# Optimization experiments

Hardware: AMD Instinct MI355X
Metric: run time of the kernel (lower is better)

Reference implementation:

```python
import jax, jax.numpy as jnp
import numpy as np

N, M, B = 2048, 2048, 1
D, H, DQK, DV = 1024, 16, 64, 64
OFFSET = 0
PARAM_SCALE = 0.02  # keeps logits in a sane range (original uses plain randn)


def setup_inputs() -> dict:
    key = jax.random.key(0)
    ks = jax.random.split(key, 7)
    return {
        "x_q": jax.random.normal(ks[0], (N, B, D), jnp.float32),
        "x_kv": jax.random.normal(ks[1], (M, B, D), jnp.float32),
        "to_q": jax.random.normal(ks[2], (DQK, H, D), jnp.float32) * PARAM_SCALE,
        "to_k": jax.random.normal(ks[3], (DQK, H, D), jnp.float32) * PARAM_SCALE,
        "to_v": jax.random.normal(ks[4], (DV, H, D), jnp.float32) * PARAM_SCALE,
        "to_out": jax.random.normal(ks[5], (D, DV, H), jnp.float32) * PARAM_SCALE,
        "for_pos_enc": jax.random.normal(ks[6], (DQK, H, D), jnp.float32) * PARAM_SCALE,
    }


def _sincos(n, m, offset, d_x_kv, dtype):
    # relative distances i - j + offset range over [offset-(m-1), offset+(n-1)]
    r = jnp.arange(offset - (m - 1), offset + (n - 1) + 1, dtype=dtype)  # [R], R=n+m-1
    inv_freq = 1.0 / (10000.0 ** (jnp.arange(0.0, d_x_kv, 2.0, dtype=dtype) / d_x_kv))
    phases = r[:, None] * inv_freq[None, :]  # [R, d/2]
    return jnp.concatenate([jnp.sin(phases), jnp.cos(phases)], axis=-1)  # [R, d]


def reference(x_q, x_kv, to_q, to_k, to_v, to_out, for_pos_enc):
    n, b, _ = x_q.shape
    m = x_kv.shape[0]
    # q: [n, d_qk, b, h]
    q = jnp.einsum('dhb,nab->ndah', to_q, x_q)
    # content logits: [n, m, b, h]
    k = jnp.einsum('dhc,mac->mdah', to_k, x_kv)
    content = jnp.einsum('ndah,mdah->nmah', q, k)
    # relative positional encoding (same math as pos_enc[dists - min] then einsum,
    # but logits computed per relative position then gathered -> no [n,m,d,h] blowup)
    sincos = _sincos(n, m, OFFSET, x_kv.shape[-1], x_q.dtype)  # [R, d_x_kv]
    pe_rel = jnp.einsum('dhb,rb->rdh', for_pos_enc, sincos)    # [R, d_qk, h]
    pl_rel = jnp.einsum('ndah,rdh->nrah', q, pe_rel)            # [n, R, b, h]
    idx = jnp.arange(n)[:, None] - jnp.arange(m)[None, :] + (m - 1)  # dists - dists.min()
    position = pl_rel[jnp.arange(n)[:, None], idx]               # [n, m, b, h]
    logits = content + position
    # causal mask: True above diagonal shifted by 1+offset
    mask = jnp.triu(jnp.ones((n, m), bool), 1 + OFFSET)
    logits = jnp.where(mask[:, :, None, None], -jnp.inf, logits)
    weights = jax.nn.softmax(logits, axis=1)                     # softmax over m
    v = jnp.einsum('chb,mab->mach', to_v, x_kv)                  # [m, b, dv, h]
    ctx = jnp.einsum('nmah,mach->nach', weights, v)              # [n, b, dv, h]
    out = jnp.einsum('dch,nach->nad', to_out, ctx)               # [n, b, d]
    return out
```

## Files before the change

kernel.cpp:

```cpp
#include <hip/hip_runtime.h>
#include <hip/hip_bf16.h>

#define N_Q   2048
#define M_KV  2048
#define DIM   1024
#define NH    16
#define DHEAD 64
#define KDIM  1024
#define PEROWS 2112
#define PEBUF  2176

typedef __attribute__((ext_vector_type(8))) __bf16 bf16x8;
typedef __attribute__((ext_vector_type(4))) float  f32x4;

typedef __attribute__((address_space(1))) const unsigned char gbyte_t;
typedef __attribute__((address_space(3))) unsigned char lbyte_t;

__device__ __forceinline__ unsigned short f2bf(float f) {
  union { float f; unsigned u; } v; v.f = f;
  unsigned u = v.u;
  u = u + 0x7fffu + ((u >> 16) & 1u);
  return (unsigned short)(u >> 16);
}

#define PREP_A 524288
#define PREP_B 1048576
#define PREP_C 2097152
#define PREP_D 2359296
#define PREP_E 2916352
__global__ __launch_bounds__(256) void prep_kernel(
    const float* __restrict__ x_q, const float* __restrict__ x_kv,
    const float* __restrict__ to_q, const float* __restrict__ to_k,
    const float* __restrict__ to_v, const float* __restrict__ to_pe,
    const float* __restrict__ to_out,
    unsigned short* __restrict__ xq_bf, unsigned short* __restrict__ xkv_bf,
    unsigned short* __restrict__ wq_bf, unsigned short* __restrict__ wkv_bf,
    unsigned short* __restrict__ wp_bf, unsigned short* __restrict__ wo_bf,
    unsigned short* __restrict__ sc_bf) {
  int gid = blockIdx.x * 256 + threadIdx.x;
  if (gid < PREP_B) {
    const float* src = (gid < PREP_A) ? x_q : x_kv;
    unsigned short* dst = (gid < PREP_A) ? xq_bf : xkv_bf;
    int e4 = (gid < PREP_A ? gid : gid - PREP_A) * 4;
    float4 v = *(const float4*)(src + e4);
    ushort4 o = { f2bf(v.x), f2bf(v.y), f2bf(v.z), f2bf(v.w) };
    *(ushort4*)(dst + e4) = o;
  } else if (gid < PREP_C) {
    int e = gid - PREP_B;
    int which = e >> 18, inner = e & 262143;
    int e4 = inner * 4;
    int j = e4 >> 10, b = e4 & 1023;
    int d = j & 63, h = j >> 6;
    const float* w = (which == 0) ? to_q : (which == 1) ? to_k : (which == 2) ? to_v : to_pe;
    unsigned short* o = (which == 0) ? wq_bf : (which == 1) ? wkv_bf
                       : (which == 2) ? (wkv_bf + (size_t)DIM * DIM) : wp_bf;
    float4 v = *(const float4*)(w + (size_t)(d * NH + h) * DIM + b);
    ushort4 u = { f2bf(v.x), f2bf(v.y), f2bf(v.z), f2bf(v.w) };
    *(ushort4*)(o + e4) = u;
  } else if (gid < PREP_D) {
    int e4 = (gid - PREP_C) * 4;
    int dd = e4 >> 10, jc = e4 & 1023;
    int c = jc & 63, h = jc >> 6;
    const float* base = to_out + (size_t)(dd * DHEAD + c) * NH + h;
    ushort4 u = { f2bf(base[0]), f2bf(base[16]), f2bf(base[32]), f2bf(base[48]) };
    *(ushort4*)(wo_bf + e4) = u;
  } else if (gid < PREP_E) {
    int e = gid - PREP_D;
    int r = e >> 8, t8 = e & 255;
    float ph0base = (float)(r - 63);
    unsigned short ss[2], cc[2];
    #pragma unroll
    for (int i = 0; i < 2; ++i) {
      int k2 = t8 * 2 + i;
      float invf = __expf((float)k2 * (-9.210340371976184f / 512.0f));
      float s, c;
      __sincosf(ph0base * invf, &s, &c);
      ss[i] = f2bf(s); cc[i] = f2bf(c);
    }
    unsigned short* row = sc_bf + (size_t)r * DIM;
    *(unsigned int*)(row + t8 * 2)       = (unsigned)ss[0] | ((unsigned)ss[1] << 16);
    *(unsigned int*)(row + t8 * 2 + 512) = (unsigned)cc[0] | ((unsigned)cc[1] << 16);
  }
}

__global__ __launch_bounds__(256) void gemm_in_kernel(
    const unsigned short* __restrict__ xq, const unsigned short* __restrict__ xkv,
    const unsigned short* __restrict__ sc,
    const unsigned short* __restrict__ wq, const unsigned short* __restrict__ wkv,
    const unsigned short* __restrict__ wp,
    unsigned short* __restrict__ qout, unsigned short* __restrict__ kout,
    unsigned short* __restrict__ vtout, unsigned short* __restrict__ peout) {
  int bid0 = (int)blockIdx.x;
  int bid  = (bid0 & 7) * 130 + (bid0 >> 3);
  const unsigned short *A, *B; unsigned short *C1, *C2;
  int Mr, maxBrow, mode, ax, by;
  if (bid < 256)      { int t = bid;       ax = t & 15; by = t >> 4; A = xq;  B = wq;  C1 = qout;  C2 = nullptr; Mr = N_Q;    maxBrow = DIM - 1;     mode = 1; }
  else if (bid < 768) { int t = bid - 256; ax = t & 15; by = t >> 4; A = xkv; B = wkv; C1 = kout;  C2 = vtout;   Mr = M_KV;   maxBrow = 2 * DIM - 1; mode = 3; }
  else                { int t = bid - 768; ax = t % 17; by = t / 17; A = sc;  B = wp;  C1 = peout; C2 = nullptr; Mr = PEROWS; maxBrow = DIM - 1;     mode = 1; }

  __shared__ unsigned short As[2][128][64];
  __shared__ unsigned short Bs[2][64][64];
  int tid  = threadIdx.x;
  int wave = tid >> 6, lane = tid & 63;
  int g = lane >> 4, r16 = lane & 15;
  int arow0 = ax * 128;
  int brow0 = by * 64;
  int amax  = Mr - 1;

  auto stage = [&](int buf, int kt) {
    #pragma unroll
    for (int n = 0; n < 4; ++n) {
      int seg  = wave * 4 + n;
      int rloc = seg * 8 + (lane >> 3);
      int cbyte = ((lane & 7) << 4) ^ ((rloc & 7) << 4);
      int grow = min(arow0 + rloc, amax);
      const unsigned short* gp = A + (size_t)grow * KDIM + kt + (cbyte >> 1);
      __builtin_amdgcn_global_load_lds((gbyte_t*)(const void*)gp,
                                       (lbyte_t*)(void*)&As[buf][seg * 8][0], 16, 0, 0);
    }
    #pragma unroll
    for (int n = 0; n < 2; ++n) {
      int seg  = wave * 2 + n;
      int rloc = seg * 8 + (lane >> 3);
      int cbyte = ((lane & 7) << 4) ^ ((rloc & 7) << 4);
      int grow = min(brow0 + rloc, maxBrow);
      const unsigned short* gp = B + (size_t)grow * KDIM + kt + (cbyte >> 1);
      __builtin_amdgcn_global_load_lds((gbyte_t*)(const void*)gp,
                                       (lbyte_t*)(void*)&Bs[buf][seg * 8][0], 16, 0, 0);
    }
  };

  f32x4 acc[2][4];
  #pragma unroll
  for (int i = 0; i < 2; ++i)
    #pragma unroll
    for (int j = 0; j < 4; ++j) acc[i][j] = (f32x4){0,0,0,0};

  stage(0, 0);
  asm volatile("s_waitcnt vmcnt(0)" ::: "memory");
  __syncthreads();

  int buf = 0;
  for (int t = 0; t < 16; ++t) {
    if (t < 15) stage(buf ^ 1, (t + 1) * 64);

    bf16x8 af[2][2], bfr[4][2];
    #pragma unroll
    for (int i = 0; i < 2; ++i)
      #pragma unroll
      for (int kk = 0; kk < 2; ++kk) {
        int r = wave * 32 + i * 16 + r16;
        int cb = ((kk << 6) | (g << 4)) ^ ((r & 7) << 4);
        af[i][kk] = *(const bf16x8*)((const char*)&As[buf][r][0] + cb);
      }
    #pragma unroll
    for (int j = 0; j < 4; ++j)
      #pragma unroll
      for (int kk = 0; kk < 2; ++kk) {
        int r = j * 16 + r16;
        int cb = ((kk << 6) | (g << 4)) ^ ((r & 7) << 4);
        bfr[j][kk] = *(const bf16x8*)((const char*)&Bs[buf][r][0] + cb);
      }
    __builtin_amdgcn_s_setprio(1);
    #pragma unroll
    for (int kk = 0; kk < 2; ++kk)
      #pragma unroll
      for (int i = 0; i < 2; ++i)
        #pragma unroll
        for (int j = 0; j < 4; ++j)
          acc[i][j] = __builtin_amdgcn_mfma_f32_16x16x32_bf16(af[i][kk], bfr[j][kk], acc[i][j], 0, 0, 0);
    __builtin_amdgcn_s_setprio(0);

    if (t < 15) {
      asm volatile("s_waitcnt vmcnt(0)" ::: "memory");
      __syncthreads();
      buf ^= 1;
    }
  }

  #pragma unroll
  for (int i = 0; i < 2; ++i)
    #pragma unroll
    for (int j = 0; j < 4; ++j)
      #pragma unroll
      for (int rr = 0; rr < 4; ++rr) {
        int row = arow0 + wave * 32 + i * 16 + g * 4 + rr;
        int col = brow0 + j * 16 + r16;
        float v = acc[i][j][rr];
        if (mode == 1) {
          if (row < Mr) C1[(size_t)row * 1024 + col] = f2bf(v);
        } else {
          if (col < 1024) C1[(size_t)row * 1024 + col] = f2bf(v);
          else            C2[(size_t)(col - 1024) * M_KV + row] = f2bf(v);
        }
      }
}

__global__ __launch_bounds__(256) void gemm_out_kernel(
    const unsigned short* __restrict__ A, const unsigned short* __restrict__ B,
    float* __restrict__ C1) {
  __shared__ unsigned short As[2][64][64];
  __shared__ unsigned short Bs[2][64][64];
  int tid  = threadIdx.x;
  int wave = tid >> 6, lane = tid & 63;
  int wr = wave >> 1, wc = wave & 1;
  int g = lane >> 4, r16 = lane & 15;
  int arow0 = blockIdx.x * 64;
  int brow0 = blockIdx.y * 64;

  auto stage = [&](int buf, int kt) {
    #pragma unroll
    for (int n = 0; n < 2; ++n) {
      int seg  = wave * 2 + n;
      int rloc = seg * 8 + (lane >> 3);
      int cbyte = ((lane & 7) << 4) ^ ((rloc & 7) << 4);
      const unsigned short* gpA = A + (size_t)(arow0 + rloc) * KDIM + kt + (cbyte >> 1);
      __builtin_amdgcn_global_load_lds((gbyte_t*)(const void*)gpA,
                                       (lbyte_t*)(void*)&As[buf][seg * 8][0], 16, 0, 0);
      const unsigned short* gpB = B + (size_t)(brow0 + rloc) * KDIM + kt + (cbyte >> 1);
      __builtin_amdgcn_global_load_lds((gbyte_t*)(const void*)gpB,
                                       (lbyte_t*)(void*)&Bs[buf][seg * 8][0], 16, 0, 0);
    }
  };

  f32x4 acc[2][2] = {{{0,0,0,0},{0,0,0,0}},{{0,0,0,0},{0,0,0,0}}};

  stage(0, 0);
  asm volatile("s_waitcnt vmcnt(0)" ::: "memory");
  __syncthreads();

  int buf = 0;
  for (int t = 0; t < 16; ++t) {
    if (t < 15) stage(buf ^ 1, (t + 1) * 64);
    bf16x8 af[2][2], bfr[2][2];
    #pragma unroll
    for (int i = 0; i < 2; ++i)
      #pragma unroll
      for (int kk = 0; kk < 2; ++kk) {
        int r = wr * 32 + i * 16 + r16;
        int cb = ((kk << 6) | (g << 4)) ^ ((r & 7) << 4);
        af[i][kk] = *(const bf16x8*)((const char*)&As[buf][r][0] + cb);
      }
    #pragma unroll
    for (int j = 0; j < 2; ++j)
      #pragma unroll
      for (int kk = 0; kk < 2; ++kk) {
        int r = wc * 32 + j * 16 + r16;
        int cb = ((kk << 6) | (g << 4)) ^ ((r & 7) << 4);
        bfr[j][kk] = *(const bf16x8*)((const char*)&Bs[buf][r][0] + cb);
      }
    __builtin_amdgcn_s_setprio(1);
    #pragma unroll
    for (int kk = 0; kk < 2; ++kk)
      #pragma unroll
      for (int i = 0; i < 2; ++i)
        #pragma unroll
        for (int j = 0; j < 2; ++j)
          acc[i][j] = __builtin_amdgcn_mfma_f32_16x16x32_bf16(af[i][kk], bfr[j][kk], acc[i][j], 0, 0, 0);
    __builtin_amdgcn_s_setprio(0);
    if (t < 15) {
      asm volatile("s_waitcnt vmcnt(0)" ::: "memory");
      __syncthreads();
      buf ^= 1;
    }
  }

  #pragma unroll
  for (int i = 0; i < 2; ++i)
    #pragma unroll
    for (int j = 0; j < 2; ++j)
      #pragma unroll
      for (int rr = 0; rr < 4; ++rr) {
        int row = arow0 + wr * 32 + i * 16 + g * 4 + rr;
        int col = brow0 + wc * 32 + j * 16 + r16;
        C1[(size_t)row * 1024 + col] = acc[i][j][rr];
      }
}

__global__ __launch_bounds__(256, 2) void attn_mfma_kernel(
    const unsigned short* __restrict__ qb, const unsigned short* __restrict__ kb,
    const unsigned short* __restrict__ vt, const unsigned short* __restrict__ pe,
    unsigned short* __restrict__ ctx, float* __restrict__ part) {
  int ord  = (int)blockIdx.x;
  int h    = ord & 15;
  int widx = 79 - (ord >> 4);
  int b, c;
  if (widx < 8)       { b = widx;                                  c = 0; }
  else if (widx < 24) { int t2 = widx - 8;  b = 8  + (t2 >> 1);    c = t2 & 1; }
  else if (widx < 48) { int t2 = widx - 24; int q3 = t2 / 3; b = 16 + q3; c = t2 - 3 * q3; }
  else                { int t2 = widx - 48; b = 24 + (t2 >> 2);    c = t2 & 3; }
  int n0   = b * 64;
  int nc   = (b < 8) ? 1 : (b >> 3) + 1;
  int t0   = c * 8;
  int tend = min(t0 + 8, b + 1);

  int wave = threadIdx.x >> 6;
  int lane = threadIdx.x & 63;
  int g    = lane >> 4;
  int r16  = lane & 15;

  __shared__ unsigned short Ks[2][64][64];
  __shared__ unsigned short Vs[2][64][64];
  __shared__ unsigned short PEs[2][128][64];
  __shared__ unsigned short W_lds[4][16][72];

  const unsigned short* qrow = qb + (size_t)(n0 + wave * 16 + r16) * DIM + h * 64 + g * 8;
  bf16x8 aq0 = *(const bf16x8*)(qrow);
  bf16x8 aq1 = *(const bf16x8*)(qrow + 32);

  union { unsigned short u[8]; bf16x8 v; } one_u;
  #pragma unroll
  for (int i = 0; i < 8; ++i) one_u.u[i] = 0x3F80;
  bf16x8 ones = one_u.v;

  f32x4 acc[4] = {{0,0,0,0},{0,0,0,0},{0,0,0,0},{0,0,0,0}};
  f32x4 lacc = {0,0,0,0};

  auto stage = [&](int bufn, int tilen) {
    int m0n = tilen * 64;
    int prb = n0 - m0n;
    #pragma unroll
    for (int n = 0; n < 2; ++n) {
      int seg  = wave * 2 + n;
      int rloc = seg * 8 + (lane >> 3);
      int cbyte = ((lane & 7) << 4) ^ ((rloc & 7) << 4);
      const unsigned short* gpk = kb + (size_t)(m0n + rloc) * KDIM + h * 64 + (cbyte >> 1);
      __builtin_amdgcn_global_load_lds((gbyte_t*)(const void*)gpk,
                                       (lbyte_t*)(void*)&Ks[bufn][seg * 8][0], 16, 0, 0);
      const unsigned short* gpv = vt + (size_t)(h * 64 + rloc) * M_KV + m0n + (cbyte >> 1);
      __builtin_amdgcn_global_load_lds((gbyte_t*)(const void*)gpv,
                                       (lbyte_t*)(void*)&Vs[bufn][seg * 8][0], 16, 0, 0);
    }
    #pragma unroll
    for (int n = 0; n < 4; ++n) {
      int seg  = wave * 4 + n;
      int rloc = seg * 8 + (lane >> 3);
      int cbyte = ((lane & 7) << 4) ^ ((rloc & 7) << 4);
      const unsigned short* gpp = pe + (size_t)(prb + rloc) * KDIM + h * 64 + (cbyte >> 1);
      __builtin_amdgcn_global_load_lds((gbyte_t*)(const void*)gpp,
                                       (lbyte_t*)(void*)&PEs[bufn][seg * 8][0], 16, 0, 0);
    }
  };

  int srcl[4]; bool hi_sel[4];
  #pragma unroll
  for (int rr = 0; rr < 4; ++rr) {
    srcl[rr]   = (g << 4) | ((g * 4 + rr + 63 - r16) & 15);
    hi_sel[rr] = (g * 4 + rr) > r16;
  }
  int sw = (r16 & 7) << 4;

  stage(0, t0);
  asm volatile("s_waitcnt vmcnt(0)" ::: "memory");
  __syncthreads();

  int buf = 0;
  for (int tile = t0; tile < tend; ++tile) {
    int m0 = tile * 64;
    if (tile + 1 < tend) stage(buf ^ 1, tile + 1);

    f32x4 s[4];
    __builtin_amdgcn_s_setprio(1);
    #pragma unroll
    for (int ct = 0; ct < 4; ++ct) {
      const char* kbase = (const char*)&Ks[buf][ct * 16 + r16][0];
      bf16x8 k0 = *(const bf16x8*)(kbase + (((g << 4)) ^ sw));
      bf16x8 k1 = *(const bf16x8*)(kbase + ((64 | (g << 4)) ^ sw));
      f32x4 z = {0,0,0,0};
      z = __builtin_amdgcn_mfma_f32_16x16x32_bf16(aq0, k0, z, 0, 0, 0);
      z = __builtin_amdgcn_mfma_f32_16x16x32_bf16(aq1, k1, z, 0, 0, 0);
      s[ct] = z;
    }

    f32x4 z2[5];
    #pragma unroll
    for (int cp = 0; cp < 5; ++cp) {
      const char* pbase = (const char*)&PEs[buf][wave * 16 + cp * 16 + r16][0];
      bf16x8 p0 = *(const bf16x8*)(pbase + (((g << 4)) ^ sw));
      bf16x8 p1 = *(const bf16x8*)(pbase + ((64 | (g << 4)) ^ sw));
      f32x4 z = {0,0,0,0};
      z = __builtin_amdgcn_mfma_f32_16x16x32_bf16(aq0, p0, z, 0, 0, 0);
      z = __builtin_amdgcn_mfma_f32_16x16x32_bf16(aq1, p1, z, 0, 0, 0);
      z2[cp] = z;
    }
    __builtin_amdgcn_s_setprio(0);

    bool diag = (m0 == n0);
    #pragma unroll
    for (int ct = 0; ct < 4; ++ct) {
      #pragma unroll
      for (int rr = 0; rr < 4; ++rr) {
        float vhi = __shfl(z2[4 - ct][rr], srcl[rr], 64);
        float vlo = __shfl(z2[3 - ct][rr], srcl[rr], 64);
        float p   = hi_sel[rr] ? vhi : vlo;
        int il = g * 4 + rr;
        int it = wave * 16 + il;
        int jt = ct * 16 + r16;
        float val = s[ct][rr] + p;
        if (diag && jt > it) val = -1e30f;
        s[ct][rr] = __expf(val);
      }
    }

    #pragma unroll
    for (int ct = 0; ct < 4; ++ct)
      #pragma unroll
      for (int rr = 0; rr < 4; ++rr)
        W_lds[wave][g * 4 + rr][ct * 16 + r16] = f2bf(s[ct][rr]);
    bf16x8 aw0 = *(const bf16x8*)(&W_lds[wave][r16][g * 8]);
    bf16x8 aw1 = *(const bf16x8*)(&W_lds[wave][r16][g * 8 + 32]);

    __builtin_amdgcn_s_setprio(1);
    #pragma unroll
    for (int ct = 0; ct < 4; ++ct) {
      const char* vbase = (const char*)&Vs[buf][ct * 16 + r16][0];
      bf16x8 v0 = *(const bf16x8*)(vbase + (((g << 4)) ^ sw));
      bf16x8 v1 = *(const bf16x8*)(vbase + ((64 | (g << 4)) ^ sw));
      f32x4 a = acc[ct];
      a = __builtin_amdgcn_mfma_f32_16x16x32_bf16(aw0, v0, a, 0, 0, 0);
      a = __builtin_amdgcn_mfma_f32_16x16x32_bf16(aw1, v1, a, 0, 0, 0);
      acc[ct] = a;
    }
    lacc = __builtin_amdgcn_mfma_f32_16x16x32_bf16(aw0, ones, lacc, 0, 0, 0);
    lacc = __builtin_amdgcn_mfma_f32_16x16x32_bf16(aw1, ones, lacc, 0, 0, 0);
    __builtin_amdgcn_s_setprio(0);

    asm volatile("s_waitcnt vmcnt(0)" ::: "memory");
    __syncthreads();
    buf ^= 1;
  }

  if (nc == 1) {
    #pragma unroll
    for (int rr = 0; rr < 4; ++rr) {
      float inv = 1.0f / lacc[rr];
      #pragma unroll
      for (int ct = 0; ct < 4; ++ct) {
        int row = n0 + wave * 16 + g * 4 + rr;
        ctx[(size_t)row * DIM + h * 64 + ct * 16 + r16] = f2bf(acc[ct][rr] * inv);
      }
    }
  } else {
    float* slot = part + ((size_t)((b - 8) * 16 + h) * 4 + c) * (64 * 68);
    #pragma unroll
    for (int ct = 0; ct < 4; ++ct)
      #pragma unroll
      for (int rr = 0; rr < 4; ++rr) {
        int row = wave * 16 + g * 4 + rr;
        slot[row * 68 + ct * 16 + r16] = acc[ct][rr];
      }
    if (r16 == 0) {
      #pragma unroll
      for (int rr = 0; rr < 4; ++rr) {
        int row = wave * 16 + g * 4 + rr;
        slot[row * 68 + 64] = lacc[rr];
      }
    }
  }
}

__global__ __launch_bounds__(256) void combine_kernel(const float* __restrict__ part,
                                                      unsigned short* __restrict__ ctx) {
  int bb = blockIdx.x;
  int h  = blockIdx.y;
  int b  = bb + 8;
  int nc = (b >> 3) + 1;
  int t  = threadIdx.x;
  int row = t >> 2, q = t & 3;
  const float* base = part + ((size_t)(bb * 16 + h) * 4) * (64 * 68) + row * 68;
  float lstar = 0.0f;
  for (int c2 = 0; c2 < nc; ++c2) lstar += base[c2 * 4352 + 64];
  float inv = 1.0f / lstar;
  for (int cc = 0; cc < 16; ++cc) {
    int col = q * 16 + cc;
    float o = 0.0f;
    for (int c2 = 0; c2 < nc; ++c2) o += base[c2 * 4352 + col];
    ctx[(size_t)(b * 64 + row) * DIM + h * 64 + col] = f2bf(o * inv);
  }
}

extern "C" void kernel_launch(void* const* d_in, const int* in_sizes, int n_in,
                              void* d_out, int out_size, void* d_ws, size_t ws_size,
                              hipStream_t stream) {
  const float* x_q    = (const float*)d_in[0];
  const float* x_kv   = (const float*)d_in[1];
  const float* to_q   = (const float*)d_in[2];
  const float* to_k   = (const float*)d_in[3];
  const float* to_v   = (const float*)d_in[4];
  const float* to_out = (const float*)d_in[5];
  const float* to_pe  = (const float*)d_in[6];

  char* ws = (char*)d_ws;
  size_t off = 0;
  auto alloc = [&](size_t bytes) -> char* {
    char* p = ws + off;
    off += (bytes + 255) & ~(size_t)255;
    return p;
  };

  unsigned short* xq_bf  = (unsigned short*)alloc((size_t)N_Q  * DIM * 2);
  unsigned short* xkv_bf = (unsigned short*)alloc((size_t)M_KV * DIM * 2);
  unsigned short* wq_bf  = (unsigned short*)alloc((size_t)DIM * DIM * 2);
  unsigned short* wkv_bf = (unsigned short*)alloc((size_t)2 * DIM * DIM * 2);
  unsigned short* wp_bf  = (unsigned short*)alloc((size_t)DIM * DIM * 2);
  unsigned short* wo_bf  = (unsigned short*)alloc((size_t)DIM * DIM * 2);
  unsigned short* sc_bf  = (unsigned short*)alloc((size_t)PEBUF * DIM * 2);
  unsigned short* q_bf   = (unsigned short*)alloc((size_t)N_Q  * DIM * 2);
  unsigned short* k_bf   = (unsigned short*)alloc((size_t)M_KV * DIM * 2);
  unsigned short* vt_bf  = (unsigned short*)alloc((size_t)DIM * M_KV * 2);
  unsigned short* pe_bf  = (unsigned short*)alloc((size_t)PEBUF * DIM * 2);
  unsigned short* ctx_bf = (unsigned short*)alloc((size_t)N_Q * DIM * 2);
  float*          part   = (float*)alloc((size_t)24 * 16 * 4 * 64 * 68 * 4);

  prep_kernel<<<11392, 256, 0, stream>>>(x_q, x_kv, to_q, to_k, to_v, to_pe, to_out,
                                         xq_bf, xkv_bf, wq_bf, wkv_bf, wp_bf, wo_bf, sc_bf);

  gemm_in_kernel<<<1040, 256, 0, stream>>>(xq_bf, xkv_bf, sc_bf, wq_bf, wkv_bf, wp_bf,
                                           q_bf, k_bf, vt_bf, pe_bf);

  attn_mfma_kernel<<<1280, 256, 0, stream>>>(q_bf, k_bf, vt_bf, pe_bf, ctx_bf, part);
  combine_kernel<<<dim3(24, NH), 256, 0, stream>>>(part, ctx_bf);

  gemm_out_kernel<<<dim3(32, 16), 256, 0, stream>>>(ctx_bf, wo_bf, (float*)d_out);
}
```

Measured before the change: 135.4 us.

## Triple-buffer LDS staging in input/output projection GEMMs with partial vmcnt waits

Both projection GEMM kernels move from double to triple buffered LDS staging, prefetching two K-tiles ahead. Waits become partial (vmcnt of one stage's loads still in flight) instead of draining all loads each iteration, and __syncthreads is replaced with a raw s_barrier plus a sched_barrier. The goal is to hide global-load latency behind MFMA work. In exchange LDS use per block grows by half, which may lower occupancy. Correctness depends on the vmcnt counts matching the number of loads issued per stage.

```diff
diff --git a/kernel.cpp b/kernel.cpp
--- a/kernel.cpp
+++ b/kernel.cpp
@@ -98,8 +98,8 @@
   else if (bid < 768) { int t = bid - 256; ax = t & 15; by = t >> 4; A = xkv; B = wkv; C1 = kout;  C2 = vtout;   Mr = M_KV;   maxBrow = 2 * DIM - 1; mode = 3; }
   else                { int t = bid - 768; ax = t % 17; by = t / 17; A = sc;  B = wp;  C1 = peout; C2 = nullptr; Mr = PEROWS; maxBrow = DIM - 1;     mode = 1; }
 
-  __shared__ unsigned short As[2][128][64];
-  __shared__ unsigned short Bs[2][64][64];
+  __shared__ unsigned short As[3][128][64];
+  __shared__ unsigned short Bs[3][64][64];
   int tid  = threadIdx.x;
   int wave = tid >> 6, lane = tid & 63;
   int g = lane >> 4, r16 = lane & 15;
@@ -137,12 +137,17 @@
     for (int j = 0; j < 4; ++j) acc[i][j] = (f32x4){0,0,0,0};
 
   stage(0, 0);
-  asm volatile("s_waitcnt vmcnt(0)" ::: "memory");
-  __syncthreads();
-
-  int buf = 0;
+  stage(1, 64);
+  asm volatile("s_waitcnt vmcnt(6)" ::: "memory");
+  __builtin_amdgcn_s_barrier();
+  __builtin_amdgcn_sched_barrier(0);
+
+  int bcur = 0;
   for (int t = 0; t < 16; ++t) {
-    if (t < 15) stage(buf ^ 1, (t + 1) * 64);
+    if (t + 2 < 16) {
+      int bstage = bcur + 2; if (bstage >= 3) bstage -= 3;
+      stage(bstage, (t + 2) * 64);
+    }
 
     bf16x8 af[2][2], bfr[4][2];
     #pragma unroll
@@ -151,7 +156,7 @@
       for (int kk = 0; kk < 2; ++kk) {
         int r = wave * 32 + i * 16 + r16;
         int cb = ((kk << 6) | (g << 4)) ^ ((r & 7) << 4);
-        af[i][kk] = *(const bf16x8*)((const char*)&As[buf][r][0] + cb);
+        af[i][kk] = *(const bf16x8*)((const char*)&As[bcur][r][0] + cb);
       }
     #pragma unroll
     for (int j = 0; j < 4; ++j)
@@ -159,7 +164,7 @@
       for (int kk = 0; kk < 2; ++kk) {
         int r = j * 16 + r16;
         int cb = ((kk << 6) | (g << 4)) ^ ((r & 7) << 4);
-        bfr[j][kk] = *(const bf16x8*)((const char*)&Bs[buf][r][0] + cb);
+        bfr[j][kk] = *(const bf16x8*)((const char*)&Bs[bcur][r][0] + cb);
       }
     __builtin_amdgcn_s_setprio(1);
     #pragma unroll
@@ -171,10 +176,12 @@
           acc[i][j] = __builtin_amdgcn_mfma_f32_16x16x32_bf16(af[i][kk], bfr[j][kk], acc[i][j], 0, 0, 0);
     __builtin_amdgcn_s_setprio(0);
 
-    if (t < 15) {
-      asm volatile("s_waitcnt vmcnt(0)" ::: "memory");
-      __syncthreads();
-      buf ^= 1;
+    if (t + 1 < 16) {
+      if (t + 2 < 16) asm volatile("s_waitcnt vmcnt(6)" ::: "memory");
+      else            asm volatile("s_waitcnt vmcnt(0)" ::: "memory");
+      __builtin_amdgcn_s_barrier();
+      __builtin_amdgcn_sched_barrier(0);
+      bcur = (bcur == 2) ? 0 : bcur + 1;
     }
   }
 
@@ -199,8 +206,8 @@
 __global__ __launch_bounds__(256) void gemm_out_kernel(
     const unsigned short* __restrict__ A, const unsigned short* __restrict__ B,
     float* __restrict__ C1) {
-  __shared__ unsigned short As[2][64][64];
-  __shared__ unsigned short Bs[2][64][64];
+  __shared__ unsigned short As[3][64][64];
+  __shared__ unsigned short Bs[3][64][64];
   int tid  = threadIdx.x;
   int wave = tid >> 6, lane = tid & 63;
   int wr = wave >> 1, wc = wave & 1;
@@ -226,12 +233,17 @@
   f32x4 acc[2][2] = {{{0,0,0,0},{0,0,0,0}},{{0,0,0,0},{0,0,0,0}}};
 
   stage(0, 0);
-  asm volatile("s_waitcnt vmcnt(0)" ::: "memory");
-  __syncthreads();
-
-  int buf = 0;
+  stage(1, 64);
+  asm volatile("s_waitcnt vmcnt(4)" ::: "memory");
+  __builtin_amdgcn_s_barrier();
+  __builtin_amdgcn_sched_barrier(0);
+
+  int bcur = 0;
   for (int t = 0; t < 16; ++t) {
-    if (t < 15) stage(buf ^ 1, (t + 1) * 64);
+    if (t + 2 < 16) {
+      int bstage = bcur + 2; if (bstage >= 3) bstage -= 3;
+      stage(bstage, (t + 2) * 64);
+    }
     bf16x8 af[2][2], bfr[2][2];
     #pragma unroll
     for (int i = 0; i < 2; ++i)
@@ -239,7 +251,7 @@
       for (int kk = 0; kk < 2; ++kk) {
         int r = wr * 32 + i * 16 + r16;
         int cb = ((kk << 6) | (g << 4)) ^ ((r & 7) << 4);
-        af[i][kk] = *(const bf16x8*)((const char*)&As[buf][r][0] + cb);
+        af[i][kk] = *(const bf16x8*)((const char*)&As[bcur][r][0] + cb);
       }
     #pragma unroll
     for (int j = 0; j < 2; ++j)
@@ -247,7 +259,7 @@
       for (int kk = 0; kk < 2; ++kk) {
         int r = wc * 32 + j * 16 + r16;
         int cb = ((kk << 6) | (g << 4)) ^ ((r & 7) << 4);
-        bfr[j][kk] = *(const bf16x8*)((const char*)&Bs[buf][r][0] + cb);
+        bfr[j][kk] = *(const bf16x8*)((const char*)&Bs[bcur][r][0] + cb);
       }
     __builtin_amdgcn_s_setprio(1);
     #pragma unroll
@@ -258,10 +270,12 @@
         for (int j = 0; j < 2; ++j)
           acc[i][j] = __builtin_amdgcn_mfma_f32_16x16x32_bf16(af[i][kk], bfr[j][kk], acc[i][j], 0, 0, 0);
     __builtin_amdgcn_s_setprio(0);
-    if (t < 15) {
-      asm volatile("s_waitcnt vmcnt(0)" ::: "memory");
-      __syncthreads();
-      buf ^= 1;
+    if (t + 1 < 16) {
+      if (t + 2 < 16) asm volatile("s_waitcnt vmcnt(4)" ::: "memory");
+      else            asm volatile("s_waitcnt vmcnt(0)" ::: "memory");
+      __builtin_amdgcn_s_barrier();
+      __builtin_amdgcn_sched_barrier(0);
+      bcur = (bcur == 2) ? 0 : bcur + 1;
     }
   }
 
```

After: 142.9 us. 5.5% more time.
